# Kernel tuning notes

Measured on AMD Instinct MI355X. Metric: run time of the kernel, lower is better.

Reference implementation:

```python
import jax, jax.numpy as jnp
import numpy as np

B, S, H = 4, 2048, 768          # batch, seq, hidden
NH, HD = 12, 64                 # heads, head dim
R = 4                           # channel_shrink_ratio
LH, LHD = H // R, HD // R       # layout hidden (192), layout head dim (16)


def setup_inputs() -> dict:
    key = jax.random.key(0)
    ks = jax.random.split(key, 14)
    s = 0.02
    return {
        "hidden_states": jax.random.normal(ks[0], (B, S, H), jnp.float32),
        "layout_inputs": jax.random.normal(ks[1], (B, S, LH), jnp.float32),
        # text-stream projections (stored as [in, out], i.e. torch weight transposed)
        "Wq": jax.random.normal(ks[2], (H, H), jnp.float32) * s,
        "bq": jnp.zeros((H,), jnp.float32),
        "Wk": jax.random.normal(ks[3], (H, H), jnp.float32) * s,
        "bk": jnp.zeros((H,), jnp.float32),
        "Wv": jax.random.normal(ks[4], (H, H), jnp.float32) * s,
        "bv": jnp.zeros((H,), jnp.float32),
        # layout-stream projections
        "lWq": jax.random.normal(ks[5], (LH, LH), jnp.float32) * s,
        "lbq": jnp.zeros((LH,), jnp.float32),
        "lWk": jax.random.normal(ks[6], (LH, LH), jnp.float32) * s,
        "lbk": jnp.zeros((LH,), jnp.float32),
        "lWv": jax.random.normal(ks[7], (LH, LH), jnp.float32) * s,
        "lbv": jnp.zeros((LH,), jnp.float32),
    }


def _heads(x, w, b, hd):
    # [B,S,D_in] @ [D_in,D_out] -> [B, NH, S, hd]
    y = x @ w + b
    return y.reshape(x.shape[0], x.shape[1], NH, hd).transpose(0, 2, 1, 3)


def reference(hidden_states, layout_inputs, Wq, bq, Wk, bk, Wv, bv,
              lWq, lbq, lWk, lbk, lWv, lbv):
    q = _heads(hidden_states, Wq, bq, HD)
    k = _heads(hidden_states, Wk, bk, HD)
    v = _heads(hidden_states, Wv, bv, HD)
    lq = _heads(layout_inputs, lWq, lbq, LHD)
    lk = _heads(layout_inputs, lWk, lbk, LHD)
    lv = _heads(layout_inputs, lWv, lbv, LHD)

    # two QK^T score matrices, scaled then cross-added (both streams see the sum)
    scores = jnp.einsum('bhqd,bhkd->bhqk', q, k) / np.float32(HD) ** 0.5
    lscores = jnp.einsum('bhqd,bhkd->bhqk', lq, lk) / np.float32(LHD) ** 0.5
    combined = scores + lscores  # identical for both streams (no mask path)

    probs = jax.nn.softmax(combined, axis=-1)
    lprobs = jax.nn.softmax(combined, axis=-1)

    ctx = jnp.einsum('bhqk,bhkd->bhqd', probs, v)
    lctx = jnp.einsum('bhqk,bhkd->bhqd', lprobs, lv)

    ctx = ctx.transpose(0, 2, 1, 3).reshape(B, S, H)
    lctx = lctx.transpose(0, 2, 1, 3).reshape(B, S, LH)
    return ctx, lctx
```

## Files before the change

### kernel.cpp

```cpp
#include <hip/hip_runtime.h>
#include <cstdint>
#include <cstddef>

#define NB 4
#define NS 2048
#define NHH 12
#define DH 80
#define HT 768
#define HL 192

typedef __bf16 bf16x8 __attribute__((ext_vector_type(8)));
typedef _Float16 f16x8 __attribute__((ext_vector_type(8)));
typedef _Float16 f16x4 __attribute__((ext_vector_type(4)));
typedef _Float16 f16x2 __attribute__((ext_vector_type(2)));
typedef float f32x4 __attribute__((ext_vector_type(4)));
typedef float f32x16 __attribute__((ext_vector_type(16)));
typedef unsigned short u16x4 __attribute__((ext_vector_type(4)));

__device__ __forceinline__ unsigned short bfc(float f) {
  __bf16 b = (__bf16)f;
  return __builtin_bit_cast(unsigned short, b);
}
__device__ __forceinline__ unsigned short f16c(float f) {
  _Float16 h = (_Float16)f;
  return __builtin_bit_cast(unsigned short, h);
}

__device__ __forceinline__ f32x4 mfma_bf16_k32(bf16x8 a, bf16x8 b, f32x4 c) {
  return __builtin_amdgcn_mfma_f32_16x16x32_bf16(a, b, c, 0, 0, 0);
}
__device__ __forceinline__ f32x16 mfma_bf16_32(bf16x8 a, bf16x8 b, f32x16 c) {
  return __builtin_amdgcn_mfma_f32_32x32x16_bf16(a, b, c, 0, 0, 0);
}
__device__ __forceinline__ f32x16 mfma_f16_32(f16x8 a, f16x8 b, f32x16 c) {
  return __builtin_amdgcn_mfma_f32_32x32x16_f16(a, b, c, 0, 0, 0);
}

__device__ __forceinline__ f16x2 pk_f16(float a, float b) {
  return __builtin_bit_cast(f16x2, __builtin_amdgcn_cvt_pkrtz(a, b));
}

__device__ __forceinline__ void gl_lds(const unsigned short* g, unsigned short* l) {
  __builtin_amdgcn_global_load_lds(
      (const __attribute__((address_space(1))) uint32_t*)g,
      (__attribute__((address_space(3))) uint32_t*)l, 16, 0, 0);
}

__global__ __launch_bounds__(256) void k_prep(
    const float* __restrict__ hs, const float* __restrict__ li,
    const float* __restrict__ Wq, const float* __restrict__ Wk, const float* __restrict__ Wv,
    const float* __restrict__ lWq, const float* __restrict__ lWk, const float* __restrict__ lWv,
    unsigned short* __restrict__ Xb, unsigned short* __restrict__ Xlb,
    unsigned short* __restrict__ WtQ, unsigned short* __restrict__ WtK,
    unsigned short* __restrict__ WtV, unsigned short* __restrict__ WtLQ,
    unsigned short* __restrict__ WtLK, unsigned short* __restrict__ WtLV) {
  __shared__ float Ts[32][33];
  int blk = blockIdx.x, tid = threadIdx.x;
  if (blk < 7680) {
    const float* src; unsigned short* dst; int i;
    if (blk < 6144) { src = hs; dst = Xb;  i = blk * 256 + tid; }
    else            { src = li; dst = Xlb; i = (blk - 6144) * 256 + tid; }
    float4 v = *(const float4*)(src + (size_t)i * 4);
    u16x4 o; o[0] = bfc(v.x); o[1] = bfc(v.y); o[2] = bfc(v.z); o[3] = bfc(v.w);
    *(u16x4*)(dst + (size_t)i * 4) = o;
  } else {
    const float* w; unsigned short* wt; int t, K;
    if (blk < 9408) {
      int b2 = blk - 7680; int m = b2 / 576; t = b2 - m * 576; K = 768;
      w  = (m == 0) ? Wq  : (m == 1) ? Wk  : Wv;
      wt = (m == 0) ? WtQ : (m == 1) ? WtK : WtV;
    } else {
      int b2 = blk - 9408; int m = b2 / 36; t = b2 - m * 36; K = 192;
      w  = (m == 0) ? lWq  : (m == 1) ? lWk  : lWv;
      wt = (m == 0) ? WtLQ : (m == 1) ? WtLK : WtLV;
    }
    int TB = K >> 5;
    int kb = t / TB, nb = t - kb * TB;
    int tx = tid & 31, ty = tid >> 5;
#pragma unroll
    for (int j = 0; j < 4; ++j)
      Ts[ty + j * 8][tx] = w[(size_t)(kb * 32 + ty + j * 8) * K + nb * 32 + tx];
    __syncthreads();
#pragma unroll
    for (int j = 0; j < 4; ++j)
      wt[(size_t)(nb * 32 + ty + j * 8) * K + kb * 32 + tx] = bfc(Ts[tx][ty + j * 8]);
  }
}

struct ProjArgs {
  const unsigned short* Wt[3];
  const float* bias[3];
  unsigned short* dst[3];
  float scale[3];
  int mode[3];
};

template<int NT>
__global__ __launch_bounds__(256, 4) void k_proj(
    const unsigned short* __restrict__ Xb, ProjArgs pa,
    int K, int hdshift, int dofs) {
  constexpr int BN = NT * 16;
  __shared__ unsigned short Xs[128 * 72];
  __shared__ unsigned short Ws[BN * 72];
  int z = blockIdx.z;
  const unsigned short* Wt = pa.Wt[z];
  int m0 = blockIdx.x * 128, n0 = blockIdx.y * BN;
  int tid = threadIdx.x;
  int lane = tid & 63, wave = tid >> 6, quad = lane >> 4, l16 = lane & 15;

  f32x4 acc[2][NT];
#pragma unroll
  for (int mt = 0; mt < 2; ++mt)
#pragma unroll
    for (int nt = 0; nt < NT; ++nt) {
      acc[mt][nt][0] = 0.f; acc[mt][nt][1] = 0.f;
      acc[mt][nt][2] = 0.f; acc[mt][nt][3] = 0.f;
    }

  for (int kk = 0; kk < K; kk += 64) {
    constexpr int XCH = 128 * 9;
#pragma unroll
    for (int p = 0; p < (XCH + 255) / 256; ++p) {
      int i = p * 256 + tid;
      if (i < XCH) {
        int r = i / 9, c = i - r * 9;
        gl_lds(Xb + (size_t)(m0 + r) * K + kk + (c == 8 ? 0 : c * 8), Xs + i * 8);
      }
    }
    constexpr int WCH = BN * 9;
#pragma unroll
    for (int p = 0; p < (WCH + 255) / 256; ++p) {
      int i = p * 256 + tid;
      if (i < WCH) {
        int r = i / 9, c = i - r * 9;
        gl_lds(Wt + (size_t)(n0 + r) * K + kk + (c == 8 ? 0 : c * 8), Ws + i * 8);
      }
    }
    __syncthreads();

#pragma unroll
    for (int kc = 0; kc < 2; ++kc) {
      bf16x8 a0 = *(const bf16x8*)&Xs[(wave * 32 + l16) * 72 + kc * 32 + quad * 8];
      bf16x8 a1 = *(const bf16x8*)&Xs[(wave * 32 + 16 + l16) * 72 + kc * 32 + quad * 8];
#pragma unroll
      for (int nt = 0; nt < NT; ++nt) {
        bf16x8 b = *(const bf16x8*)&Ws[(nt * 16 + l16) * 72 + kc * 32 + quad * 8];
        acc[0][nt] = mfma_bf16_k32(a0, b, acc[0][nt]);
        acc[1][nt] = mfma_bf16_k32(a1, b, acc[1][nt]);
      }
    }
    __syncthreads();
  }

  const float* bias = pa.bias[z];
  unsigned short* dst = pa.dst[z];
  float scale = pa.scale[z];
  int mode = pa.mode[z];
  int hdm = (1 << hdshift) - 1;
#pragma unroll
  for (int mt = 0; mt < 2; ++mt) {
#pragma unroll
    for (int nt = 0; nt < NT; ++nt) {
      int n = n0 + nt * 16 + l16;
      float bv = bias[n];
      int mbase = m0 + wave * 32 + mt * 16 + quad * 4;
      int h = n >> hdshift, d = n & hdm;
      if (mode == 0) {
#pragma unroll
        for (int r = 0; r < 4; ++r) {
          int m = mbase + r;
          int b = m >> 11, s = m & (NS - 1);
          dst[((size_t)(b * NHH + h) * NS + s) * DH + dofs + d] =
              bfc((acc[mt][nt][r] + bv) * scale);
        }
      } else {
        int b = mbase >> 11, s = mbase & (NS - 1);
        u16x4 pk;
#pragma unroll
        for (int r = 0; r < 4; ++r) pk[r] = f16c((acc[mt][nt][r] + bv) * scale);
        *(u16x4*)(dst + ((size_t)(b * NHH + h) * DH + dofs + d) * NS + s) = pk;
      }
    }
  }
}

__global__ __launch_bounds__(256, 3) void k_attn(
    const unsigned short* __restrict__ Qg, const unsigned short* __restrict__ Kg,
    const unsigned short* __restrict__ Vg,
    float* __restrict__ outT, float* __restrict__ outL) {
  __shared__ unsigned short KT[2][64 * 88];
  __shared__ unsigned short VT[2][96 * 72];

  int tid = threadIdx.x;
  int lane = tid & 63, w = tid >> 6, h = lane >> 5, l32 = lane & 31;
  int bh = blockIdx.x, qb = blockIdx.y;
  int bb = bh / NHH, hh = bh - bb * NHH;
  int q0 = qb * 128;

  const unsigned short* kg0 = Kg + (size_t)bh * NS * DH;
  const unsigned short* vg0 = Vg + (size_t)bh * DH * NS;

  for (int i = tid; i < 2304; i += 256) {
    int b = i / 1152, j = i - b * 1152;
    VT[b][80 * 72 + j] = (j < 72) ? (unsigned short)0x3C00 : (unsigned short)0;
  }

  bf16x8 qf[5];
  {
    const unsigned short* qrow = Qg + ((size_t)bh * NS + q0 + w * 32 + l32) * DH;
#pragma unroll
    for (int kc = 0; kc < 5; ++kc)
      qf[kc] = *(const bf16x8*)(qrow + kc * 16 + h * 8);
  }

  f32x16 o[3];
#pragma unroll
  for (int vt = 0; vt < 3; ++vt)
#pragma unroll
    for (int r = 0; r < 16; ++r) o[vt][r] = 0.f;

  auto stage = [&](int buf, int kt) {
    const unsigned short* kb = kg0 + (size_t)kt * 64 * DH;
    unsigned short* dk = &KT[buf][0];
#pragma unroll
    for (int p = 0; p < 3; ++p) {
      int i = p * 256 + tid;
      if (i < 704) {
        int r = i / 11, c = i - r * 11;
        int rs = ((((r >> 2) ^ (r >> 3)) & 1) ? (r ^ 12) : r);
        gl_lds(kb + (size_t)rs * DH + (c == 10 ? 0 : c * 8), dk + i * 8);
      }
    }
    int k0 = kt * 64;
    unsigned short* dv = &VT[buf][0];
#pragma unroll
    for (int p = 0; p < 3; ++p) {
      int i = p * 256 + tid;
      if (i < 720) {
        int r = i / 9, c = i - r * 9;
        gl_lds((c == 8) ? vg0 : (vg0 + (size_t)r * NS + k0 + c * 8), dv + i * 8);
      }
    }
  };

  stage(0, 0);

  for (int kt = 0; kt < 32; ++kt) {
    int cur = kt & 1;
    __syncthreads();
    if (kt + 1 < 32) stage(cur ^ 1, kt + 1);

    const unsigned short* Kc = &KT[cur][0];
    const unsigned short* Vc = &VT[cur][0];

    f32x16 st[2];
#pragma unroll
    for (int t = 0; t < 2; ++t)
#pragma unroll
      for (int r = 0; r < 16; ++r) st[t][r] = 0.f;

#pragma unroll
    for (int kc = 0; kc < 5; ++kc) {
#pragma unroll
      for (int t = 0; t < 2; ++t) {
        bf16x8 a = *(const bf16x8*)&Kc[(t * 32 + l32) * 88 + kc * 16 + h * 8];
        st[t] = mfma_bf16_32(a, qf[kc], st[t]);
      }
    }

#pragma unroll
    for (int t = 0; t < 2; ++t) {
#pragma unroll
      for (int p = 0; p < 2; ++p) {
        union { f16x8 v; f16x2 h2[4]; } u;
#pragma unroll
        for (int j2 = 0; j2 < 4; ++j2)
          u.h2[j2] = pk_f16(__expf(st[t][8 * p + 2 * j2]),
                            __expf(st[t][8 * p + 2 * j2 + 1]));
        int s = 2 * t + p;
#pragma unroll
        for (int vt = 0; vt < 3; ++vt) {
          f16x8 va = *(const f16x8*)&Vc[(vt * 32 + l32) * 72 + s * 16 + h * 8];
          o[vt] = mfma_f16_32(va, u.v, o[vt]);
        }
      }
    }
  }

  float rsum = __shfl(o[2][8], l32);
  float inv = 1.0f / rsum;
  int s = q0 + w * 32 + l32;
  float* rowT = outT + ((size_t)bb * NS + s) * HT + hh * 64 + 4 * h;
#pragma unroll
  for (int vt = 0; vt < 2; ++vt)
#pragma unroll
    for (int g = 0; g < 4; ++g) {
      float4 v4;
      v4.x = o[vt][4 * g + 0] * inv; v4.y = o[vt][4 * g + 1] * inv;
      v4.z = o[vt][4 * g + 2] * inv; v4.w = o[vt][4 * g + 3] * inv;
      *(float4*)(rowT + vt * 32 + 8 * g) = v4;
    }
  float* rowL = outL + ((size_t)bb * NS + s) * HL + hh * 16 + 4 * h;
#pragma unroll
  for (int g = 0; g < 2; ++g) {
    float4 v4;
    v4.x = o[2][4 * g + 0] * inv; v4.y = o[2][4 * g + 1] * inv;
    v4.z = o[2][4 * g + 2] * inv; v4.w = o[2][4 * g + 3] * inv;
    *(float4*)(rowL + 8 * g) = v4;
  }
}

extern "C" void kernel_launch(void* const* d_in, const int* in_sizes, int n_in,
                              void* d_out, int out_size, void* d_ws, size_t ws_size,
                              hipStream_t stream) {
  const float* hs  = (const float*)d_in[0];
  const float* li  = (const float*)d_in[1];
  const float* Wq  = (const float*)d_in[2];
  const float* bq  = (const float*)d_in[3];
  const float* Wk  = (const float*)d_in[4];
  const float* bk  = (const float*)d_in[5];
  const float* Wv  = (const float*)d_in[6];
  const float* bv  = (const float*)d_in[7];
  const float* lWq = (const float*)d_in[8];
  const float* lbq = (const float*)d_in[9];
  const float* lWk = (const float*)d_in[10];
  const float* lbk = (const float*)d_in[11];
  const float* lWv = (const float*)d_in[12];
  const float* lbv = (const float*)d_in[13];

  char* ws = (char*)d_ws;
  size_t off = 0;
  auto alloc = [&](size_t bytes) {
    char* p = ws + off;
    off += (bytes + 255) & ~(size_t)255;
    return (unsigned short*)p;
  };
  unsigned short* Xb   = alloc((size_t)8192 * 768 * 2);
  unsigned short* Xlb  = alloc((size_t)8192 * 192 * 2);
  unsigned short* WtQ  = alloc((size_t)768 * 768 * 2);
  unsigned short* WtK  = alloc((size_t)768 * 768 * 2);
  unsigned short* WtV  = alloc((size_t)768 * 768 * 2);
  unsigned short* WtLQ = alloc((size_t)192 * 192 * 2);
  unsigned short* WtLK = alloc((size_t)192 * 192 * 2);
  unsigned short* WtLV = alloc((size_t)192 * 192 * 2);
  unsigned short* Qs   = alloc((size_t)NB * NHH * NS * DH * 2);
  unsigned short* Ks   = alloc((size_t)NB * NHH * NS * DH * 2);
  unsigned short* Vs   = alloc((size_t)NB * NHH * NS * DH * 2 + 256);

  k_prep<<<9516, 256, 0, stream>>>(hs, li, Wq, Wk, Wv, lWq, lWk, lWv,
                                   Xb, Xlb, WtQ, WtK, WtV, WtLQ, WtLK, WtLV);

  const float s8 = 0.35355339059327373f;
  const float s4 = 0.5f;
  {
    ProjArgs pa;
    pa.Wt[0] = WtQ; pa.Wt[1] = WtK; pa.Wt[2] = WtV;
    pa.bias[0] = bq; pa.bias[1] = bk; pa.bias[2] = bv;
    pa.dst[0] = Qs; pa.dst[1] = Ks; pa.dst[2] = Vs;
    pa.scale[0] = s8; pa.scale[1] = s8; pa.scale[2] = 1.f;
    pa.mode[0] = 0; pa.mode[1] = 0; pa.mode[2] = 1;
    k_proj<8><<<dim3(64, 6, 3), 256, 0, stream>>>(Xb, pa, 768, 6, 0);
  }
  {
    ProjArgs pa;
    pa.Wt[0] = WtLQ; pa.Wt[1] = WtLK; pa.Wt[2] = WtLV;
    pa.bias[0] = lbq; pa.bias[1] = lbk; pa.bias[2] = lbv;
    pa.dst[0] = Qs; pa.dst[1] = Ks; pa.dst[2] = Vs;
    pa.scale[0] = s4; pa.scale[1] = s4; pa.scale[2] = 1.f;
    pa.mode[0] = 0; pa.mode[1] = 0; pa.mode[2] = 1;
    k_proj<4><<<dim3(64, 3, 3), 256, 0, stream>>>(Xlb, pa, 192, 4, 64);
  }
  float* outT = (float*)d_out;
  float* outL = outT + (size_t)NB * NS * HT;
  k_attn<<<dim3(48, 16), 256, 0, stream>>>(Qs, Ks, Vs, outT, outL);
}
```

Baseline: 238.4 us.

## Double query tiles per attention wave, fold log2e into Q, vectorize projection stores

The attention kernel now runs with 128 threads, and each wave handles two 32-row query tiles. This lets every K and V fragment read from LDS feed twice as many MFMAs. The log2(e) factor is folded into the Q projection scale so the softmax can use the raw exp2 instruction in place of __expf. The Q/K projection swaps the MFMA operands so each lane owns contiguous head-dim outputs, which allows 4-wide packed stores and a vector bias load. The trade-off is more registers per wave and fewer waves per block for hiding latency.

Measured after the change: 378.9 us. 1.59x slower.

```diff
diff --git a/kernel.cpp b/kernel.cpp
--- a/kernel.cpp
+++ b/kernel.cpp
@@ -11,7 +11,6 @@
 
 typedef __bf16 bf16x8 __attribute__((ext_vector_type(8)));
 typedef _Float16 f16x8 __attribute__((ext_vector_type(8)));
-typedef _Float16 f16x4 __attribute__((ext_vector_type(4)));
 typedef _Float16 f16x2 __attribute__((ext_vector_type(2)));
 typedef float f32x4 __attribute__((ext_vector_type(4)));
 typedef float f32x16 __attribute__((ext_vector_type(16)));
@@ -24,6 +23,10 @@
 __device__ __forceinline__ unsigned short f16c(float f) {
   _Float16 h = (_Float16)f;
   return __builtin_bit_cast(unsigned short, h);
+}
+
+__device__ __forceinline__ float ex2(float x) {
+  return __builtin_amdgcn_exp2f(x);
 }
 
 __device__ __forceinline__ f32x4 mfma_bf16_k32(bf16x8 a, bf16x8 b, f32x4 c) {
@@ -104,6 +107,7 @@
   __shared__ unsigned short Ws[BN * 72];
   int z = blockIdx.z;
   const unsigned short* Wt = pa.Wt[z];
+  const bool swp = (pa.mode[z] == 0);
   int m0 = blockIdx.x * 128, n0 = blockIdx.y * BN;
   int tid = threadIdx.x;
   int lane = tid & 63, wave = tid >> 6, quad = lane >> 4, l16 = lane & 15;
@@ -140,13 +144,22 @@
 
 #pragma unroll
     for (int kc = 0; kc < 2; ++kc) {
-      bf16x8 a0 = *(const bf16x8*)&Xs[(wave * 32 + l16) * 72 + kc * 32 + quad * 8];
-      bf16x8 a1 = *(const bf16x8*)&Xs[(wave * 32 + 16 + l16) * 72 + kc * 32 + quad * 8];
-#pragma unroll
-      for (int nt = 0; nt < NT; ++nt) {
-        bf16x8 b = *(const bf16x8*)&Ws[(nt * 16 + l16) * 72 + kc * 32 + quad * 8];
-        acc[0][nt] = mfma_bf16_k32(a0, b, acc[0][nt]);
-        acc[1][nt] = mfma_bf16_k32(a1, b, acc[1][nt]);
+      bf16x8 x0 = *(const bf16x8*)&Xs[(wave * 32 + l16) * 72 + kc * 32 + quad * 8];
+      bf16x8 x1 = *(const bf16x8*)&Xs[(wave * 32 + 16 + l16) * 72 + kc * 32 + quad * 8];
+      if (swp) {
+#pragma unroll
+        for (int nt = 0; nt < NT; ++nt) {
+          bf16x8 wf = *(const bf16x8*)&Ws[(nt * 16 + l16) * 72 + kc * 32 + quad * 8];
+          acc[0][nt] = mfma_bf16_k32(wf, x0, acc[0][nt]);
+          acc[1][nt] = mfma_bf16_k32(wf, x1, acc[1][nt]);
+        }
+      } else {
+#pragma unroll
+        for (int nt = 0; nt < NT; ++nt) {
+          bf16x8 wf = *(const bf16x8*)&Ws[(nt * 16 + l16) * 72 + kc * 32 + quad * 8];
+          acc[0][nt] = mfma_bf16_k32(x0, wf, acc[0][nt]);
+          acc[1][nt] = mfma_bf16_k32(x1, wf, acc[1][nt]);
+        }
       }
     }
     __syncthreads();
@@ -155,25 +168,34 @@
   const float* bias = pa.bias[z];
   unsigned short* dst = pa.dst[z];
   float scale = pa.scale[z];
-  int mode = pa.mode[z];
   int hdm = (1 << hdshift) - 1;
-#pragma unroll
-  for (int mt = 0; mt < 2; ++mt) {
-#pragma unroll
-    for (int nt = 0; nt < NT; ++nt) {
-      int n = n0 + nt * 16 + l16;
-      float bv = bias[n];
-      int mbase = m0 + wave * 32 + mt * 16 + quad * 4;
-      int h = n >> hdshift, d = n & hdm;
-      if (mode == 0) {
-#pragma unroll
-        for (int r = 0; r < 4; ++r) {
-          int m = mbase + r;
-          int b = m >> 11, s = m & (NS - 1);
-          dst[((size_t)(b * NHH + h) * NS + s) * DH + dofs + d] =
-              bfc((acc[mt][nt][r] + bv) * scale);
-        }
-      } else {
+  if (swp) {
+#pragma unroll
+    for (int mt = 0; mt < 2; ++mt) {
+      int m_l = m0 + wave * 32 + mt * 16 + l16;
+      int b = m_l >> 11, s = m_l & (NS - 1);
+      size_t rowbase = (size_t)b * NHH * NS * DH + (size_t)s * DH + dofs;
+#pragma unroll
+      for (int nt = 0; nt < NT; ++nt) {
+        int dl = nt * 16 + quad * 4;
+        int n = n0 + dl;
+        f32x4 b4 = *(const f32x4*)(bias + n);
+        int h = n >> hdshift, d = n & hdm;
+        u16x4 pk;
+#pragma unroll
+        for (int r = 0; r < 4; ++r) pk[r] = bfc((acc[mt][nt][r] + b4[r]) * scale);
+        *(u16x4*)(dst + rowbase + (size_t)h * NS * DH + d) = pk;
+      }
+    }
+  } else {
+#pragma unroll
+    for (int mt = 0; mt < 2; ++mt) {
+#pragma unroll
+      for (int nt = 0; nt < NT; ++nt) {
+        int n = n0 + nt * 16 + l16;
+        float bv = bias[n];
+        int mbase = m0 + wave * 32 + mt * 16 + quad * 4;
+        int h = n >> hdshift, d = n & hdm;
         int b = mbase >> 11, s = mbase & (NS - 1);
         u16x4 pk;
 #pragma unroll
@@ -184,7 +206,7 @@
   }
 }
 
-__global__ __launch_bounds__(256, 3) void k_attn(
+__global__ __launch_bounds__(128, 2) void k_attn(
     const unsigned short* __restrict__ Qg, const unsigned short* __restrict__ Kg,
     const unsigned short* __restrict__ Vg,
     float* __restrict__ outT, float* __restrict__ outL) {
@@ -200,31 +222,35 @@
   const unsigned short* kg0 = Kg + (size_t)bh * NS * DH;
   const unsigned short* vg0 = Vg + (size_t)bh * DH * NS;
 
-  for (int i = tid; i < 2304; i += 256) {
+  for (int i = tid; i < 2304; i += 128) {
     int b = i / 1152, j = i - b * 1152;
     VT[b][80 * 72 + j] = (j < 72) ? (unsigned short)0x3C00 : (unsigned short)0;
   }
 
-  bf16x8 qf[5];
-  {
-    const unsigned short* qrow = Qg + ((size_t)bh * NS + q0 + w * 32 + l32) * DH;
+  bf16x8 qf[2][5];
+#pragma unroll
+  for (int qt = 0; qt < 2; ++qt) {
+    const unsigned short* qrow =
+        Qg + ((size_t)bh * NS + q0 + w * 64 + qt * 32 + l32) * DH;
 #pragma unroll
     for (int kc = 0; kc < 5; ++kc)
-      qf[kc] = *(const bf16x8*)(qrow + kc * 16 + h * 8);
-  }
-
-  f32x16 o[3];
-#pragma unroll
-  for (int vt = 0; vt < 3; ++vt)
-#pragma unroll
-    for (int r = 0; r < 16; ++r) o[vt][r] = 0.f;
+      qf[qt][kc] = *(const bf16x8*)(qrow + kc * 16 + h * 8);
+  }
+
+  f32x16 o[2][3];
+#pragma unroll
+  for (int qt = 0; qt < 2; ++qt)
+#pragma unroll
+    for (int vt = 0; vt < 3; ++vt)
+#pragma unroll
+      for (int r = 0; r < 16; ++r) o[qt][vt][r] = 0.f;
 
   auto stage = [&](int buf, int kt) {
     const unsigned short* kb = kg0 + (size_t)kt * 64 * DH;
     unsigned short* dk = &KT[buf][0];
 #pragma unroll
-    for (int p = 0; p < 3; ++p) {
-      int i = p * 256 + tid;
+    for (int p = 0; p < 6; ++p) {
+      int i = p * 128 + tid;
       if (i < 704) {
         int r = i / 11, c = i - r * 11;
         int rs = ((((r >> 2) ^ (r >> 3)) & 1) ? (r ^ 12) : r);
@@ -234,8 +260,8 @@
     int k0 = kt * 64;
     unsigned short* dv = &VT[buf][0];
 #pragma unroll
-    for (int p = 0; p < 3; ++p) {
-      int i = p * 256 + tid;
+    for (int p = 0; p < 6; ++p) {
+      int i = p * 128 + tid;
       if (i < 720) {
         int r = i / 9, c = i - r * 9;
         gl_lds((c == 8) ? vg0 : (vg0 + (size_t)r * NS + k0 + c * 8), dv + i * 8);
@@ -253,18 +279,21 @@
     const unsigned short* Kc = &KT[cur][0];
     const unsigned short* Vc = &VT[cur][0];
 
-    f32x16 st[2];
-#pragma unroll
-    for (int t = 0; t < 2; ++t)
-#pragma unroll
-      for (int r = 0; r < 16; ++r) st[t][r] = 0.f;
+    f32x16 st[2][2];
+#pragma unroll
+    for (int qt = 0; qt < 2; ++qt)
+#pragma unroll
+      for (int t = 0; t < 2; ++t)
+#pragma unroll
+        for (int r = 0; r < 16; ++r) st[qt][t][r] = 0.f;
 
 #pragma unroll
     for (int kc = 0; kc < 5; ++kc) {
 #pragma unroll
       for (int t = 0; t < 2; ++t) {
         bf16x8 a = *(const bf16x8*)&Kc[(t * 32 + l32) * 88 + kc * 16 + h * 8];
-        st[t] = mfma_bf16_32(a, qf[kc], st[t]);
+        st[0][t] = mfma_bf16_32(a, qf[0][kc], st[0][t]);
+        st[1][t] = mfma_bf16_32(a, qf[1][kc], st[1][t]);
       }
     }
 
@@ -272,41 +301,50 @@
     for (int t = 0; t < 2; ++t) {
 #pragma unroll
       for (int p = 0; p < 2; ++p) {
-        union { f16x8 v; f16x2 h2[4]; } u;
-#pragma unroll
-        for (int j2 = 0; j2 < 4; ++j2)
-          u.h2[j2] = pk_f16(__expf(st[t][8 * p + 2 * j2]),
-                            __expf(st[t][8 * p + 2 * j2 + 1]));
+        f16x8 pv[2];
+#pragma unroll
+        for (int qt = 0; qt < 2; ++qt) {
+          union { f16x8 v; f16x2 h2[4]; } u;
+#pragma unroll
+          for (int j2 = 0; j2 < 4; ++j2)
+            u.h2[j2] = pk_f16(ex2(st[qt][t][8 * p + 2 * j2]),
+                              ex2(st[qt][t][8 * p + 2 * j2 + 1]));
+          pv[qt] = u.v;
+        }
         int s = 2 * t + p;
 #pragma unroll
         for (int vt = 0; vt < 3; ++vt) {
           f16x8 va = *(const f16x8*)&Vc[(vt * 32 + l32) * 72 + s * 16 + h * 8];
-          o[vt] = mfma_f16_32(va, u.v, o[vt]);
+          o[0][vt] = mfma_f16_32(va, pv[0], o[0][vt]);
+          o[1][vt] = mfma_f16_32(va, pv[1], o[1][vt]);
         }
       }
     }
   }
 
-  float rsum = __shfl(o[2][8], l32);
-  float inv = 1.0f / rsum;
-  int s = q0 + w * 32 + l32;
-  float* rowT = outT + ((size_t)bb * NS + s) * HT + hh * 64 + 4 * h;
-#pragma unroll
-  for (int vt = 0; vt < 2; ++vt)
-#pragma unroll
-    for (int g = 0; g < 4; ++g) {
+#pragma unroll
+  for (int qt = 0; qt < 2; ++qt) {
+    float rsum = __shfl(o[qt][2][8], l32);
+    float inv = 1.0f / rsum;
+    int s = q0 + w * 64 + qt * 32 + l32;
+    float* rowT = outT + ((size_t)bb * NS + s) * HT + hh * 64 + 4 * h;
+#pragma unroll
+    for (int vt = 0; vt < 2; ++vt)
+#pragma unroll
+      for (int g = 0; g < 4; ++g) {
+        float4 v4;
+        v4.x = o[qt][vt][4 * g + 0] * inv; v4.y = o[qt][vt][4 * g + 1] * inv;
+        v4.z = o[qt][vt][4 * g + 2] * inv; v4.w = o[qt][vt][4 * g + 3] * inv;
+        *(float4*)(rowT + vt * 32 + 8 * g) = v4;
+      }
+    float* rowL = outL + ((size_t)bb * NS + s) * HL + hh * 16 + 4 * h;
+#pragma unroll
+    for (int g = 0; g < 2; ++g) {
       float4 v4;
-      v4.x = o[vt][4 * g + 0] * inv; v4.y = o[vt][4 * g + 1] * inv;
-      v4.z = o[vt][4 * g + 2] * inv; v4.w = o[vt][4 * g + 3] * inv;
-      *(float4*)(rowT + vt * 32 + 8 * g) = v4;
-    }
-  float* rowL = outL + ((size_t)bb * NS + s) * HL + hh * 16 + 4 * h;
-#pragma unroll
-  for (int g = 0; g < 2; ++g) {
-    float4 v4;
-    v4.x = o[2][4 * g + 0] * inv; v4.y = o[2][4 * g + 1] * inv;
-    v4.z = o[2][4 * g + 2] * inv; v4.w = o[2][4 * g + 3] * inv;
-    *(float4*)(rowL + 8 * g) = v4;
+      v4.x = o[qt][2][4 * g + 0] * inv; v4.y = o[qt][2][4 * g + 1] * inv;
+      v4.z = o[qt][2][4 * g + 2] * inv; v4.w = o[qt][2][4 * g + 3] * inv;
+      *(float4*)(rowL + 8 * g) = v4;
+    }
   }
 }
 
@@ -350,6 +388,7 @@
   k_prep<<<9516, 256, 0, stream>>>(hs, li, Wq, Wk, Wv, lWq, lWk, lWv,
                                    Xb, Xlb, WtQ, WtK, WtV, WtLQ, WtLK, WtLV);
 
+  const float LOG2E = 1.4426950408889634f;
   const float s8 = 0.35355339059327373f;
   const float s4 = 0.5f;
   {
@@ -357,7 +396,7 @@
     pa.Wt[0] = WtQ; pa.Wt[1] = WtK; pa.Wt[2] = WtV;
     pa.bias[0] = bq; pa.bias[1] = bk; pa.bias[2] = bv;
     pa.dst[0] = Qs; pa.dst[1] = Ks; pa.dst[2] = Vs;
-    pa.scale[0] = s8; pa.scale[1] = s8; pa.scale[2] = 1.f;
+    pa.scale[0] = s8 * LOG2E; pa.scale[1] = s8; pa.scale[2] = 1.f;
     pa.mode[0] = 0; pa.mode[1] = 0; pa.mode[2] = 1;
     k_proj<8><<<dim3(64, 6, 3), 256, 0, stream>>>(Xb, pa, 768, 6, 0);
   }
@@ -366,11 +405,11 @@
     pa.Wt[0] = WtLQ; pa.Wt[1] = WtLK; pa.Wt[2] = WtLV;
     pa.bias[0] = lbq; pa.bias[1] = lbk; pa.bias[2] = lbv;
     pa.dst[0] = Qs; pa.dst[1] = Ks; pa.dst[2] = Vs;
-    pa.scale[0] = s4; pa.scale[1] = s4; pa.scale[2] = 1.f;
+    pa.scale[0] = s4 * LOG2E; pa.scale[1] = s4; pa.scale[2] = 1.f;
     pa.mode[0] = 0; pa.mode[1] = 0; pa.mode[2] = 1;
     k_proj<4><<<dim3(64, 3, 3), 256, 0, stream>>>(Xlb, pa, 192, 4, 64);
   }
   float* outT = (float*)d_out;
   float* outL = outT + (size_t)NB * NS * HT;
-  k_attn<<<dim3(48, 16), 256, 0, stream>>>(Qs, Ks, Vs, outT, outL);
-}
+  k_attn<<<dim3(48, 16), 128, 0, stream>>>(Qs, Ks, Vs, outT, outL);
+}
```
